# Performance work log

Measured on AMD Instinct MI355X. Metric: run time of the kernel, lower is better.

The kernel has to match this reference:

```python
import jax, jax.numpy as jnp
import numpy as np

N0 = 100000
N1 = 100000
K = 16
D_MODEL = 64
D_ATTN = 32
H = 4


def setup_inputs() -> dict:
    key = jax.random.key(0)
    ks = jax.random.split(key, 12)
    inp = {
        "coords0": jax.random.normal(ks[0], (N0, 3), jnp.float32),
        "coords1": jax.random.normal(ks[1], (N1, 3), jnp.float32),
        "feats0": jax.random.normal(ks[2], (N0, D_MODEL), jnp.float32),
        "feats1": jax.random.normal(ks[3], (N1, D_MODEL), jnp.float32),
        "knn_idxs": jax.random.randint(ks[4], (1, N1, K), 0, N0, jnp.int64 if jax.config.jax_enable_x64 else jnp.int32),
        # Linear params (PyTorch Linear: y = x @ W.T + b; stored here already transposed as [in, out])
        "Wq": jax.random.normal(ks[5], (D_MODEL, D_ATTN), jnp.float32) / np.sqrt(D_MODEL),
        "bq": jnp.zeros((D_ATTN,), jnp.float32),
        "Wk": jax.random.normal(ks[6], (D_MODEL + 3, D_ATTN), jnp.float32) / np.sqrt(D_MODEL + 3),
        "bk": jnp.zeros((D_ATTN,), jnp.float32),
        "Wv": jax.random.normal(ks[7], (D_MODEL + 3, D_MODEL), jnp.float32) / np.sqrt(D_MODEL + 3),
        "bv": jnp.zeros((D_MODEL,), jnp.float32),
    }
    return inp


def reference(coords0, coords1, feats0, feats1, knn_idxs, Wq, bq, Wk, bk, Wv, bv):
    idx = knn_idxs[0]  # [N1, K] neighbor indices into cloud 0
    n1, k_ = idx.shape
    dh_attn = D_ATTN // H   # per-head query/key depth
    dh_val = D_MODEL // H   # per-head value depth

    # Irregular gathers from source cloud
    g_feats = feats0[idx]                         # [N1, K, D_MODEL]
    rel = coords0[idx] - coords1[:, None, :]      # [N1, K, 3] relative coords
    kv_in = jnp.concatenate([g_feats, rel], axis=-1)  # [N1, K, D_MODEL+3]

    # Projections + head split
    q = (feats1 @ Wq + bq).reshape(n1, H, dh_attn)                    # [N1, H, dh]
    k = (kv_in @ Wk + bk).reshape(n1, k_, H, dh_attn).transpose(0, 2, 1, 3)  # [N1, H, K, dh]
    v = (kv_in @ Wv + bv).reshape(n1, k_, H, dh_val).transpose(0, 2, 1, 3)   # [N1, H, K, dv]

    # Attention over K neighbors per point
    attn = jnp.einsum('nhd,nhkd->nhk', q, k) / np.sqrt(dh_attn).astype(np.float32)
    attn = jax.nn.softmax(attn, axis=-1)          # [N1, H, K]
    out = jnp.einsum('nhk,nhkd->nhd', attn, v)    # [N1, H, dv]
    out = out.reshape(n1, -1)                     # [N1, D_MODEL]
    return out, knn_idxs
```

## Files before the change

kernel.cpp:

```cpp
#include <hip/hip_runtime.h>


using half8   = __attribute__((ext_vector_type(8))) _Float16;
using half4   = __attribute__((ext_vector_type(4))) _Float16;
using floatx4 = __attribute__((ext_vector_type(4))) float;

__global__ __launch_bounds__(256, 4) void proj_fused(
    const float* __restrict__ feats0, const float* __restrict__ feats1,
    const float* __restrict__ Wq, const float* __restrict__ bq,
    const float* __restrict__ Wk, const float* __restrict__ bk,
    const float* __restrict__ Wv, const float* __restrict__ bv,
    _Float16* __restrict__ KVh, float* __restrict__ Qf,
    int n0, int n1, int nb0)
{
    __shared__ __align__(16) _Float16 sFrag[6144];
    __shared__ __align__(16) _Float16 sOut[6144];

    const int tid  = threadIdx.x;
    const int wave = tid >> 6;
    const int lane = tid & 63;
    const int l15  = lane & 15;
    const int quad = lane >> 4;

    if ((int)blockIdx.x < nb0) {
        const int rowBase = blockIdx.x * 64;
        for (int e = tid; e < 6144; e += 256) {
            int j = e & 7, ln = (e >> 3) & 63, h = (e >> 9) & 1, t = e >> 10;
            int k = h * 32 + ((ln >> 4) * 8) + j;
            int n = t * 16 + (ln & 15);
            float v = (n < 32) ? Wk[k * 32 + n] : Wv[k * 64 + (n - 32)];
            sFrag[e] = (_Float16)v;
        }
        __syncthreads();

        const int m0   = rowBase + wave * 16;
        const int row  = m0 + l15;
        const int rowc = (row < n0) ? row : (n0 - 1);
        const floatx4* X4 = (const floatx4*)(feats0 + (size_t)rowc * 64);
        floatx4 f0 = X4[quad * 2 + 0], f1 = X4[quad * 2 + 1];
        floatx4 f2 = X4[quad * 2 + 8], f3 = X4[quad * 2 + 9];
        half8 a0, a1;
        a0[0]=(_Float16)f0.x; a0[1]=(_Float16)f0.y; a0[2]=(_Float16)f0.z; a0[3]=(_Float16)f0.w;
        a0[4]=(_Float16)f1.x; a0[5]=(_Float16)f1.y; a0[6]=(_Float16)f1.z; a0[7]=(_Float16)f1.w;
        a1[0]=(_Float16)f2.x; a1[1]=(_Float16)f2.y; a1[2]=(_Float16)f2.z; a1[3]=(_Float16)f2.w;
        a1[4]=(_Float16)f3.x; a1[5]=(_Float16)f3.y; a1[6]=(_Float16)f3.z; a1[7]=(_Float16)f3.w;

        const half8* bf = (const half8*)sFrag;
        floatx4 acc[6];
        #pragma unroll
        for (int t = 0; t < 6; t++) {
            int n = t * 16 + l15;
            float bb = (n < 32) ? bk[n] : bv[n - 32];
            acc[t] = (floatx4){bb, bb, bb, bb};
        }
        #pragma unroll
        for (int t = 0; t < 6; t++) {
            acc[t] = __builtin_amdgcn_mfma_f32_16x16x32_f16(a0, bf[(t*2+0)*64 + lane], acc[t], 0,0,0);
            acc[t] = __builtin_amdgcn_mfma_f32_16x16x32_f16(a1, bf[(t*2+1)*64 + lane], acc[t], 0,0,0);
        }

        #pragma unroll
        for (int t = 0; t < 6; t++)
            #pragma unroll
            for (int r = 0; r < 4; r++)
                sOut[(wave * 16 + quad * 4 + r) * 96 + t * 16 + l15] = (_Float16)acc[t][r];
        __syncthreads();

        const half8* so8 = (const half8*)sOut;
        half8* dst = (half8*)(KVh + (size_t)rowBase * 96);
        for (int c = tid; c < 768; c += 256) {
            int r = c / 12;
            if (rowBase + r < n0) dst[c] = so8[c];
        }
    } else {
        const int rowBase = ((int)blockIdx.x - nb0) * 64;
        for (int e = tid; e < 2048; e += 256) {
            int j = e & 7, ln = (e >> 3) & 63, h = (e >> 9) & 1, t = e >> 10;
            int k = h * 32 + ((ln >> 4) * 8) + j;
            int n = t * 16 + (ln & 15);
            sFrag[e] = (_Float16)Wq[k * 32 + n];
        }
        __syncthreads();

        const int m0   = rowBase + wave * 16;
        const int row  = m0 + l15;
        const int rowc = (row < n1) ? row : (n1 - 1);
        const floatx4* X4 = (const floatx4*)(feats1 + (size_t)rowc * 64);
        floatx4 f0 = X4[quad * 2 + 0], f1 = X4[quad * 2 + 1];
        floatx4 f2 = X4[quad * 2 + 8], f3 = X4[quad * 2 + 9];
        half8 a0, a1;
        a0[0]=(_Float16)f0.x; a0[1]=(_Float16)f0.y; a0[2]=(_Float16)f0.z; a0[3]=(_Float16)f0.w;
        a0[4]=(_Float16)f1.x; a0[5]=(_Float16)f1.y; a0[6]=(_Float16)f1.z; a0[7]=(_Float16)f1.w;
        a1[0]=(_Float16)f2.x; a1[1]=(_Float16)f2.y; a1[2]=(_Float16)f2.z; a1[3]=(_Float16)f2.w;
        a1[4]=(_Float16)f3.x; a1[5]=(_Float16)f3.y; a1[6]=(_Float16)f3.z; a1[7]=(_Float16)f3.w;

        const half8* bf = (const half8*)sFrag;
        floatx4 acc[2];
        #pragma unroll
        for (int t = 0; t < 2; t++) {
            float bb = bq[t * 16 + l15];
            acc[t] = (floatx4){bb, bb, bb, bb};
        }
        #pragma unroll
        for (int t = 0; t < 2; t++) {
            acc[t] = __builtin_amdgcn_mfma_f32_16x16x32_f16(a0, bf[(t*2+0)*64 + lane], acc[t], 0,0,0);
            acc[t] = __builtin_amdgcn_mfma_f32_16x16x32_f16(a1, bf[(t*2+1)*64 + lane], acc[t], 0,0,0);
        }
        #pragma unroll
        for (int t = 0; t < 2; t++)
            #pragma unroll
            for (int r = 0; r < 4; r++) {
                int ro = m0 + quad * 4 + r;
                if (ro < n1) Qf[(size_t)ro * 32 + t * 16 + l15] = acc[t][r];
            }
    }
}

__global__ __launch_bounds__(256, 4) void attn_kernel(
    const float* __restrict__ coords0, const float* __restrict__ coords1,
    const int*   __restrict__ knn,
    const float* __restrict__ Qf, const _Float16* __restrict__ KVh,
    const float* __restrict__ Wk, const float* __restrict__ Wv,
    float* __restrict__ out, float* __restrict__ outIdx, int n1)
{
    __shared__ __align__(16) float sQ[16][36];
    __shared__ float sWk3[3][32];
    __shared__ float sWv3[3][64];
    __shared__ float sAttn[16][4][18];
    __shared__ float sRel[16][16][3];
    __shared__ int   sIdx[16][16];

    const int tid = threadIdx.x;
    for (int e = tid; e < 288; e += 256) {
        if (e < 96) ((float*)sWk3)[e] = Wk[2048 + e];
        else        ((float*)sWv3)[e - 96] = Wv[4096 + (e - 96)];
    }
    if (tid < 128) {
        int pt = tid >> 3, c4 = tid & 7;
        int r = blockIdx.x * 16 + pt;
        if (r >= n1) r = n1 - 1;
        ((floatx4*)&sQ[pt][0])[c4] = ((const floatx4*)Qf)[(size_t)r * 8 + c4];
    }
    __syncthreads();

    const int p = tid >> 4;
    const int j = tid & 15;
    const int n = blockIdx.x * 16 + p;
    const bool valid = (n < n1);
    const int nc = valid ? n : (n1 - 1);

    const int idx = knn[nc * 16 + j];
    const half8* kr = (const half8*)(KVh + (size_t)idx * 96);
    half8 k8[4];
    #pragma unroll
    for (int h = 0; h < 4; h++) k8[h] = kr[h];

    const float r0 = coords0[idx * 3 + 0] - coords1[nc * 3 + 0];
    const float r1 = coords0[idx * 3 + 1] - coords1[nc * 3 + 1];
    const float r2 = coords0[idx * 3 + 2] - coords1[nc * 3 + 2];

    float t_own = 0.f;
    if (j < 12) {
        int c = j >> 2, h = j & 3;
        #pragma unroll
        for (int i = 0; i < 8; i++)
            t_own = fmaf(sWk3[c][h * 8 + i], sQ[p][h * 8 + i], t_own);
    }
    float tt[3][4];
    #pragma unroll
    for (int c = 0; c < 3; c++)
        #pragma unroll
        for (int h = 0; h < 4; h++)
            tt[c][h] = __shfl(t_own, c * 4 + h, 16);

    const float scale = 0.35355339059327373f;
    #pragma unroll
    for (int h = 0; h < 4; h++) {
        floatx4 q0 = ((const floatx4*)&sQ[p][0])[h * 2 + 0];
        floatx4 q1 = ((const floatx4*)&sQ[p][0])[h * 2 + 1];
        float acc = r0 * tt[0][h] + r1 * tt[1][h] + r2 * tt[2][h];
        acc = fmaf(q0.x, (float)k8[h][0], acc);
        acc = fmaf(q0.y, (float)k8[h][1], acc);
        acc = fmaf(q0.z, (float)k8[h][2], acc);
        acc = fmaf(q0.w, (float)k8[h][3], acc);
        acc = fmaf(q1.x, (float)k8[h][4], acc);
        acc = fmaf(q1.y, (float)k8[h][5], acc);
        acc = fmaf(q1.z, (float)k8[h][6], acc);
        acc = fmaf(q1.w, (float)k8[h][7], acc);
        float e = __expf(acc * scale);
        float s = e;
        s += __shfl_xor(s, 1, 16);
        s += __shfl_xor(s, 2, 16);
        s += __shfl_xor(s, 4, 16);
        s += __shfl_xor(s, 8, 16);
        sAttn[p][h][j] = e * __builtin_amdgcn_rcpf(s);
    }
    sRel[p][j][0] = r0; sRel[p][j][1] = r1; sRel[p][j][2] = r2;
    sIdx[p][j] = idx;
    if (valid) outIdx[n * 16 + j] = (float)idx;

    __syncthreads();

    const int g = j & 7;
    const int hf = j >> 3;
    const int h = g >> 1;

    int   iv[8];
    float av[8];
    #pragma unroll
    for (int s = 0; s < 8; s++) {
        iv[s] = sIdx[p][2 * s + hf];
        av[s] = sAttn[p][h][2 * s + hf];
    }
    half8 v8[8];
    #pragma unroll
    for (int s = 0; s < 8; s++)
        v8[s] = *(const half8*)(KVh + (size_t)iv[s] * 96 + 32 + g * 8);

    float acc8[8] = {0,0,0,0,0,0,0,0};
    float rb0 = 0.f, rb1 = 0.f, rb2 = 0.f;
    #pragma unroll
    for (int s = 0; s < 8; s++) {
        float a = av[s];
        #pragma unroll
        for (int i = 0; i < 8; i++)
            acc8[i] = fmaf(a, (float)v8[s][i], acc8[i]);
        rb0 = fmaf(a, sRel[p][2 * s + hf][0], rb0);
        rb1 = fmaf(a, sRel[p][2 * s + hf][1], rb1);
        rb2 = fmaf(a, sRel[p][2 * s + hf][2], rb2);
    }
    #pragma unroll
    for (int i = 0; i < 8; i++) acc8[i] += __shfl_xor(acc8[i], 8, 16);
    rb0 += __shfl_xor(rb0, 8, 16);
    rb1 += __shfl_xor(rb1, 8, 16);
    rb2 += __shfl_xor(rb2, 8, 16);

    #pragma unroll
    for (int i = 0; i < 8; i++)
        acc8[i] += rb0 * sWv3[0][8 * g + i] + rb1 * sWv3[1][8 * g + i] + rb2 * sWv3[2][8 * g + i];

    if (valid) {
        floatx4 st = { acc8[hf * 4 + 0], acc8[hf * 4 + 1], acc8[hf * 4 + 2], acc8[hf * 4 + 3] };
        ((floatx4*)out)[(size_t)n * 16 + g * 2 + hf] = st;
    }
}

extern "C" void kernel_launch(void* const* d_in, const int* in_sizes, int n_in,
                              void* d_out, int out_size, void* d_ws, size_t ws_size,
                              hipStream_t stream) {
    const float* coords0 = (const float*)d_in[0];
    const float* coords1 = (const float*)d_in[1];
    const float* feats0  = (const float*)d_in[2];
    const float* feats1  = (const float*)d_in[3];
    const int*   knn     = (const int*)d_in[4];
    const float* Wq      = (const float*)d_in[5];
    const float* bq      = (const float*)d_in[6];
    const float* Wk      = (const float*)d_in[7];
    const float* bk      = (const float*)d_in[8];
    const float* Wv      = (const float*)d_in[9];
    const float* bv      = (const float*)d_in[10];

    const int n0 = in_sizes[0] / 3;
    const int n1 = in_sizes[1] / 3;

    char* ws = (char*)d_ws;
    _Float16* KVh = (_Float16*)ws;
    float*    Qf  = (float*)(ws + (size_t)n0 * 96 * 2);

    float* out    = (float*)d_out;
    float* outIdx = out + (size_t)n1 * 64;

    const int nb0 = (n0 + 63) / 64;
    const int nb1 = (n1 + 63) / 64;

    proj_fused<<<nb0 + nb1, 256, 0, stream>>>(feats0, feats1, Wq, bq, Wk, bk, Wv, bv,
                                              KVh, Qf, n0, n1, nb0);
    attn_kernel<<<(n1 + 15) / 16, 256, 0, stream>>>(coords0, coords1, knn,
                                                    Qf, KVh, Wk, Wv, out, outIdx, n1);
}
```

Measured before the change: 200.6 us.

## Replace shared-memory attention handoff with shuffles and issue V loads early

Removes the shared-memory staging of attention weights, relative coords and neighbor indices, along with the block-wide barrier. Neighbor indices, weights and relative coordinates are now exchanged within each 16-lane group by shuffles. The V-row gathers are issued before the score and softmax computation, so their latency can overlap with the arithmetic. The cost is more shuffle instructions (seven per step for weights and coordinates) and higher register pressure from holding the eight V vectors across the softmax phase.

```diff
diff --git a/kernel.cpp b/kernel.cpp
--- a/kernel.cpp
+++ b/kernel.cpp
@@ -2,7 +2,6 @@
 
 
 using half8   = __attribute__((ext_vector_type(8))) _Float16;
-using half4   = __attribute__((ext_vector_type(4))) _Float16;
 using floatx4 = __attribute__((ext_vector_type(4))) float;
 
 __global__ __launch_bounds__(256, 4) void proj_fused(
@@ -126,9 +125,6 @@
     __shared__ __align__(16) float sQ[16][36];
     __shared__ float sWk3[3][32];
     __shared__ float sWv3[3][64];
-    __shared__ float sAttn[16][4][18];
-    __shared__ float sRel[16][16][3];
-    __shared__ int   sIdx[16][16];
 
     const int tid = threadIdx.x;
     for (int e = tid; e < 288; e += 256) {
@@ -150,84 +146,91 @@
     const int nc = valid ? n : (n1 - 1);
 
     const int idx = knn[nc * 16 + j];
+
     const half8* kr = (const half8*)(KVh + (size_t)idx * 96);
-    half8 k8[4];
-    #pragma unroll
-    for (int h = 0; h < 4; h++) k8[h] = kr[h];
+    half8 k8_0 = kr[0], k8_1 = kr[1], k8_2 = kr[2], k8_3 = kr[3];
 
     const float r0 = coords0[idx * 3 + 0] - coords1[nc * 3 + 0];
     const float r1 = coords0[idx * 3 + 1] - coords1[nc * 3 + 1];
     const float r2 = coords0[idx * 3 + 2] - coords1[nc * 3 + 2];
 
+    const int g  = j & 7;
+    const int hf = j >> 3;
+    const int h  = g >> 1;
+
+    int vIdx[8];
+    #pragma unroll
+    for (int s = 0; s < 8; s++)
+        vIdx[s] = __shfl(idx, 2 * s + hf, 16);
+    half8 v8[8];
+    #pragma unroll
+    for (int s = 0; s < 8; s++)
+        v8[s] = *(const half8*)(KVh + (size_t)vIdx[s] * 96 + 32 + g * 8);
+
     float t_own = 0.f;
     if (j < 12) {
-        int c = j >> 2, h = j & 3;
+        int c = j >> 2, h2 = j & 3;
         #pragma unroll
         for (int i = 0; i < 8; i++)
-            t_own = fmaf(sWk3[c][h * 8 + i], sQ[p][h * 8 + i], t_own);
+            t_own = fmaf(sWk3[c][h2 * 8 + i], sQ[p][h2 * 8 + i], t_own);
     }
     float tt[3][4];
     #pragma unroll
     for (int c = 0; c < 3; c++)
         #pragma unroll
-        for (int h = 0; h < 4; h++)
-            tt[c][h] = __shfl(t_own, c * 4 + h, 16);
+        for (int h2 = 0; h2 < 4; h2++)
+            tt[c][h2] = __shfl(t_own, c * 4 + h2, 16);
 
     const float scale = 0.35355339059327373f;
-    #pragma unroll
-    for (int h = 0; h < 4; h++) {
-        floatx4 q0 = ((const floatx4*)&sQ[p][0])[h * 2 + 0];
-        floatx4 q1 = ((const floatx4*)&sQ[p][0])[h * 2 + 1];
-        float acc = r0 * tt[0][h] + r1 * tt[1][h] + r2 * tt[2][h];
-        acc = fmaf(q0.x, (float)k8[h][0], acc);
-        acc = fmaf(q0.y, (float)k8[h][1], acc);
-        acc = fmaf(q0.z, (float)k8[h][2], acc);
-        acc = fmaf(q0.w, (float)k8[h][3], acc);
-        acc = fmaf(q1.x, (float)k8[h][4], acc);
-        acc = fmaf(q1.y, (float)k8[h][5], acc);
-        acc = fmaf(q1.z, (float)k8[h][6], acc);
-        acc = fmaf(q1.w, (float)k8[h][7], acc);
-        float e = __expf(acc * scale);
-        float s = e;
-        s += __shfl_xor(s, 1, 16);
-        s += __shfl_xor(s, 2, 16);
-        s += __shfl_xor(s, 4, 16);
-        s += __shfl_xor(s, 8, 16);
-        sAttn[p][h][j] = e * __builtin_amdgcn_rcpf(s);
-    }
-    sRel[p][j][0] = r0; sRel[p][j][1] = r1; sRel[p][j][2] = r2;
-    sIdx[p][j] = idx;
+    float a0, a1, a2, a3;
+    {
+        half8 k8[4] = {k8_0, k8_1, k8_2, k8_3};
+        float av[4];
+        #pragma unroll
+        for (int h2 = 0; h2 < 4; h2++) {
+            floatx4 q0 = ((const floatx4*)&sQ[p][0])[h2 * 2 + 0];
+            floatx4 q1 = ((const floatx4*)&sQ[p][0])[h2 * 2 + 1];
+            float acc = r0 * tt[0][h2] + r1 * tt[1][h2] + r2 * tt[2][h2];
+            acc = fmaf(q0.x, (float)k8[h2][0], acc);
+            acc = fmaf(q0.y, (float)k8[h2][1], acc);
+            acc = fmaf(q0.z, (float)k8[h2][2], acc);
+            acc = fmaf(q0.w, (float)k8[h2][3], acc);
+            acc = fmaf(q1.x, (float)k8[h2][4], acc);
+            acc = fmaf(q1.y, (float)k8[h2][5], acc);
+            acc = fmaf(q1.z, (float)k8[h2][6], acc);
+            acc = fmaf(q1.w, (float)k8[h2][7], acc);
+            float e = __expf(acc * scale);
+            float s = e;
+            s += __shfl_xor(s, 1, 16);
+            s += __shfl_xor(s, 2, 16);
+            s += __shfl_xor(s, 4, 16);
+            s += __shfl_xor(s, 8, 16);
+            av[h2] = e * __builtin_amdgcn_rcpf(s);
+        }
+        a0 = av[0]; a1 = av[1]; a2 = av[2]; a3 = av[3];
+    }
+
     if (valid) outIdx[n * 16 + j] = (float)idx;
-
-    __syncthreads();
-
-    const int g = j & 7;
-    const int hf = j >> 3;
-    const int h = g >> 1;
-
-    int   iv[8];
-    float av[8];
-    #pragma unroll
-    for (int s = 0; s < 8; s++) {
-        iv[s] = sIdx[p][2 * s + hf];
-        av[s] = sAttn[p][h][2 * s + hf];
-    }
-    half8 v8[8];
-    #pragma unroll
-    for (int s = 0; s < 8; s++)
-        v8[s] = *(const half8*)(KVh + (size_t)iv[s] * 96 + 32 + g * 8);
 
     float acc8[8] = {0,0,0,0,0,0,0,0};
     float rb0 = 0.f, rb1 = 0.f, rb2 = 0.f;
     #pragma unroll
     for (int s = 0; s < 8; s++) {
-        float a = av[s];
+        const int src = 2 * s + hf;
+        float t0 = __shfl(a0, src, 16);
+        float t1 = __shfl(a1, src, 16);
+        float t2 = __shfl(a2, src, 16);
+        float t3 = __shfl(a3, src, 16);
+        float av = (h == 0) ? t0 : (h == 1) ? t1 : (h == 2) ? t2 : t3;
+        float sr0 = __shfl(r0, src, 16);
+        float sr1 = __shfl(r1, src, 16);
+        float sr2 = __shfl(r2, src, 16);
         #pragma unroll
         for (int i = 0; i < 8; i++)
-            acc8[i] = fmaf(a, (float)v8[s][i], acc8[i]);
-        rb0 = fmaf(a, sRel[p][2 * s + hf][0], rb0);
-        rb1 = fmaf(a, sRel[p][2 * s + hf][1], rb1);
-        rb2 = fmaf(a, sRel[p][2 * s + hf][2], rb2);
+            acc8[i] = fmaf(av, (float)v8[s][i], acc8[i]);
+        rb0 = fmaf(av, sr0, rb0);
+        rb1 = fmaf(av, sr1, rb1);
+        rb2 = fmaf(av, sr2, rb2);
     }
     #pragma unroll
     for (int i = 0; i < 8; i++) acc8[i] += __shfl_xor(acc8[i], 8, 16);
```

After: 191.2 us. 1.05x faster.
